# Optimization experiments

Measured on AMD Instinct MI355X. Metric: run time of the kernel, lower is better.

Reference implementation:

```python
import jax, jax.numpy as jnp
import numpy as np

B, RES, C = 4, 128, 256
HW = RES * RES
H_FFT, W_FFT = RES, RES // 2 + 1
NUM_BANDS, GATE_HIDDEN = 6, 128
LN_EPS = 1e-5
FFT_NORM = 'ortho'
INIT_RANGE = 0.02


def _band_info(h_fft, w_fft, nb):
    # static radial band partition of the rFFT2 plane (matches RadialBandGate.__init__)
    yy = np.arange(h_fft, dtype=np.float32)[:, None] / max(h_fft - 1, 1)
    xx = np.arange(w_fft, dtype=np.float32)[None, :] / max(w_fft - 1, 1)
    r = np.sqrt(yy ** 2 + xx ** 2)
    r = r / (r.max() + 1e-8)
    bid = np.minimum(np.floor(r * nb), nb - 1).astype(np.int32).reshape(-1)  # (F,)
    onehot = np.zeros((bid.size, nb), dtype=np.float32)
    onehot[np.arange(bid.size), bid] = 1.0
    counts = np.maximum(onehot.sum(0), 1.0)
    return jnp.asarray(bid), jnp.asarray(onehot), jnp.asarray(counts)

BAND_ID, BAND_ONEHOT, BAND_COUNTS = _band_info(H_FFT, W_FFT, NUM_BANDS)


def setup_inputs() -> dict:
    key = jax.random.key(0)
    ks = jax.random.split(key, 16)
    return {
        'x': jax.random.normal(ks[0], (B, HW, C), jnp.float32),
        'time': jax.random.uniform(ks[1], (B,), jnp.float32),
        'w_real': jax.random.normal(ks[2], (C, C), jnp.float32) * INIT_RANGE,
        'w_imag': jax.random.normal(ks[3], (C, C), jnp.float32) * INIT_RANGE,
        'conv_w': jax.random.normal(ks[4], (C, 1, 3, 3), jnp.float32) * 0.1,  # depthwise
        'lin_w': jax.random.normal(ks[5], (C, C), jnp.float32) * 0.02,
        'lin_b': jnp.zeros((C,), jnp.float32),
        'mlp_w1': jax.random.normal(ks[6], (GATE_HIDDEN, NUM_BANDS), jnp.float32) * 0.3,
        'mlp_b1': jnp.zeros((GATE_HIDDEN,), jnp.float32),
        'mlp_w2': jax.random.normal(ks[7], (NUM_BANDS, GATE_HIDDEN), jnp.float32) * 0.1,
        'mlp_b2': jnp.zeros((NUM_BANDS,), jnp.float32),
        'norm_ww': jax.random.normal(ks[8], (C, 1), jnp.float32) * 0.02,  # ConditionalLayerNorm.weight Linear(1,dim)
        'norm_wb': jnp.ones((C,), jnp.float32),
        'norm_bw': jax.random.normal(ks[9], (C, 1), jnp.float32) * 0.02,
        'norm_bb': jnp.zeros((C,), jnp.float32),
        'kx': jnp.asarray(0.25, jnp.float32),
        'ky': jnp.asarray(0.25, jnp.float32),
    }


def _band_gate(feat, mlp_w1, mlp_b1, mlp_w2, mlp_b2):
    # feat: (B, C, F) real. scatter-add per band via one-hot matmul, mean, MLP, gather back.
    sums = jnp.einsum('bcf,fn->bcn', feat, BAND_ONEHOT)           # (B,C,NB)
    means = sums / (BAND_COUNTS + 1e-6)
    h = jax.nn.relu(jnp.einsum('bcn,hn->bch', means, mlp_w1) + mlp_b1)
    alpha_band = jax.nn.sigmoid(jnp.einsum('bch,nh->bcn', h, mlp_w2) + mlp_b2)
    return alpha_band[:, :, BAND_ID]                               # (B,C,F)


def reference(x, time, w_real, w_imag, conv_w, lin_w, lin_b,
              mlp_w1, mlp_b1, mlp_w2, mlp_b2,
              norm_ww, norm_wb, norm_bw, norm_bb, kx, ky):
    h = w = RES
    x2 = jnp.transpose(x.reshape(B, h, w, C), (0, 3, 1, 2))        # (B,C,h,w)
    Xf = jnp.fft.rfft2(x2, norm=FFT_NORM)                          # (B,C,h_fft,w_fft) complex

    # low-frequency rectangular mask (int(sigmoid(k)*dim) == floor for positive values)
    kx_i = jnp.floor(jax.nn.sigmoid(kx) * H_FFT)
    ky_i = jnp.floor(jax.nn.sigmoid(ky) * W_FFT)
    mask = ((jnp.arange(H_FFT)[:, None] < kx_i) & (jnp.arange(W_FFT)[None, :] < ky_i))
    Xf_low = Xf * mask[None, None].astype(Xf.real.dtype)

    F = H_FFT * W_FFT
    Xf_low_flat = Xf_low.reshape(B, C, F)
    W = w_real + 1j * w_imag                                       # (C,C) complex
    Xf_low_mapped = jnp.einsum('cd,bdf->bcf', W, Xf_low_flat).reshape(B, C, H_FFT, W_FFT)

    Xf_high = Xf - Xf_low
    feat_pred = jnp.abs(jnp.abs(Xf_high).reshape(B, C, F) - jnp.abs(Xf_low).reshape(B, C, F))
    alpha = _band_gate(feat_pred, mlp_w1, mlp_b1, mlp_w2, mlp_b2).reshape(B, C, H_FFT, W_FFT)

    Xf_fused = alpha * Xf_low_mapped + (1.0 - alpha) * Xf_high
    x_spec = jnp.fft.irfft2(Xf_fused, s=(h, w), norm=FFT_NORM)     # (B,C,h,w) real

    # depthwise 3x3 conv, padding=1, no bias
    xl = jax.lax.conv_general_dilated(x2, conv_w, window_strides=(1, 1), padding='SAME',
                                      feature_group_count=C,
                                      dimension_numbers=('NCHW', 'OIHW', 'NCHW'))
    # pointwise linear over channel dim
    xc = jnp.transpose((x @ lin_w.T + lin_b).reshape(B, h, w, C), (0, 3, 1, 2))

    y = jnp.transpose(x_spec + xl + xc, (0, 2, 3, 1)).reshape(B, HW, C)

    # ConditionalLayerNorm
    mean = y.mean(axis=-1, keepdims=True)
    var = (y ** 2).mean(axis=-1, keepdims=True) - mean ** 2
    yn = (y - mean) / jnp.sqrt(var + LN_EPS)
    t = time.reshape(-1, 1)                                        # (B,1)
    weight = (t @ norm_ww.T + norm_wb)[:, None, :]                 # (B,1,C)
    bias = (t @ norm_bw.T + norm_bb)[:, None, :]
    return weight * yn + bias
```

## Files before the change

### kernel.cpp

```cpp
#include <hip/hip_runtime.h>
#include <math.h>

#define B_ 4
#define C_ 256
#define RES_ 128
#define HW_ 16384
#define WF_ 65
#define F_ 8320
#define FP_ 2880

typedef __attribute__((ext_vector_type(8))) short bf16x8;
typedef __attribute__((ext_vector_type(16))) float f32x16;

__device__ __forceinline__ int brev6(int j){ return (int)(__brev((unsigned)j) >> 26); }

__device__ __forceinline__ short f2bf(float f){
  unsigned u = __float_as_uint(f);
  unsigned r = (u + 0x7FFFu + ((u>>16)&1u)) >> 16;
  return (short)r;
}

__device__ __forceinline__ bf16x8 lds_frag(const short* p){
  union { bf16x8 v; int2 d[2]; } u;
  u.d[0] = *(const int2*)p;
  u.d[1] = *(const int2*)(p+4);
  return u.v;
}
__device__ __forceinline__ void lds_store8(short* p, bf16x8 v){
  union { bf16x8 v; int2 d[2]; } u; u.v = v;
  *(int2*)p = u.d[0]; *(int2*)(p+4) = u.d[1];
}

__device__ __forceinline__ int band_of(int row, int col){
  float yy = __fdiv_rn((float)row, 127.0f);
  float xx = __fdiv_rn((float)col, 64.0f);
  float rr = __fsqrt_rn(__fadd_rn(__fmul_rn(yy,yy), __fmul_rn(xx,xx)));
  float rm = __fadd_rn(__fsqrt_rn(2.0f), 1e-8f);
  float rn = __fdiv_rn(rr, rm);
  int b = (int)floorf(__fmul_rn(rn, 6.0f));
  return b > 5 ? 5 : b;
}

__device__ __forceinline__ float sigmoidf_(float v){ return 1.0f/(1.0f+expf(-v)); }

template<int SGN>
__device__ __forceinline__ float2 wave_fft64(float2 v, const float2* stw, int lane){
  #pragma unroll
  for (int s=0; s<6; s++){
    int H = 32 >> s;
    float ox = __shfl_xor(v.x, H);
    float oy = __shfl_xor(v.y, H);
    bool hi = (lane & H) != 0;
    float2 w = stw[s];
    float ws = (SGN < 0) ? -w.y : w.y;
    float sx = v.x + ox, sy = v.y + oy;
    float dx = ox - v.x, dy = oy - v.y;
    float rx = dx*w.x - dy*ws;
    float ry = dx*ws + dy*w.x;
    v.x = hi ? rx : sx;
    v.y = hi ? ry : sy;
  }
  return v;
}

__device__ __forceinline__ void make_stage_tw(float2* stw, int lane){
  #pragma unroll
  for (int s=0; s<6; s++){
    int H = 32 >> s;
    int t = (lane & (H-1)) << s;
    float sn, cs;
    sincosf(6.283185307179586f*(float)t/64.0f, &sn, &cs);
    stw[s] = make_float2(cs, sn);
  }
}

__device__ __forceinline__ void redist2(float2 a0, float2 a1, int lane, float2& u0, float2& u1){
  int s0 = lane >> 1, s1 = s0 + 32;
  bool odd = (lane & 1) != 0;
  float t0x = __shfl(a0.x, s0), t0y = __shfl(a0.y, s0);
  float t1x = __shfl(a1.x, s0), t1y = __shfl(a1.y, s0);
  u0 = odd ? make_float2(t1x, t1y) : make_float2(t0x, t0y);
  float q0x = __shfl(a0.x, s1), q0y = __shfl(a0.y, s1);
  float q1x = __shfl(a1.x, s1), q1y = __shfl(a1.y, s1);
  u1 = odd ? make_float2(q1x, q1y) : make_float2(q0x, q0y);
}

__global__ __launch_bounds__(256) void k_transpose(const float* __restrict__ x, float* __restrict__ x2){
  __shared__ float tile[64][68];
  int b = blockIdx.z;
  int hw0 = blockIdx.x*64, c0 = blockIdx.y*64;
  int tid = threadIdx.x;
  #pragma unroll
  for (int q=0;q<4;q++){
    int p = tid + q*256;
    int hw = p >> 4, c4 = (p & 15) << 2;
    float4 v = *(const float4*)&x[((size_t)b*HW_ + hw0 + hw)*C_ + c0 + c4];
    *(float4*)&tile[hw][c4] = v;
  }
  __syncthreads();
  #pragma unroll
  for (int q=0;q<4;q++){
    int p = tid + q*256;
    int c = p >> 4, h4 = (p & 15) << 2;
    float4 v = make_float4(tile[h4][c], tile[h4+1][c], tile[h4+2][c], tile[h4+3][c]);
    *(float4*)&x2[((size_t)b*C_ + c0 + c)*HW_ + hw0 + h4] = v;
  }
}

__global__ __launch_bounds__(256) void k_counts(float* __restrict__ counts, unsigned char* __restrict__ bid_t){
  int tid = threadIdx.x;
  float acc[6] = {0,0,0,0,0,0};
  for (int p = tid; p < F_; p += 256){
    int kx = p >> 7, ky = p & 127;
    int bnd = band_of(ky, kx);
    bid_t[p] = (unsigned char)bnd;
    #pragma unroll
    for (int n=0;n<6;n++) acc[n] += (bnd==n) ? 1.0f : 0.0f;
  }
  __shared__ float red[6][256];
  #pragma unroll
  for (int n=0;n<6;n++) red[n][tid] = acc[n];
  __syncthreads();
  for (int s=128; s>0; s>>=1){
    if (tid < s){
      #pragma unroll
      for (int n=0;n<6;n++) red[n][tid] += red[n][tid+s];
    }
    __syncthreads();
  }
  if (tid < 6) counts[tid] = fmaxf(red[tid][0], 1.0f);
}

__global__ __launch_bounds__(256) void k_wbf16(const float* __restrict__ wre, const float* __restrict__ wim,
                                               const float* __restrict__ lw,
                                               short* __restrict__ Wre, short* __restrict__ Wim,
                                               short* __restrict__ WL){
  int c = blockIdx.x, tid = threadIdx.x, plane = blockIdx.y;
  int idx = c*C_ + tid;
  if (plane == 0)      Wre[idx] = f2bf(wre[idx]);
  else if (plane == 1) Wim[idx] = f2bf(wim[idx]);
  else                 WL[idx]  = f2bf(lw[idx]);
}

__global__ __launch_bounds__(512) void k_fwd(const float* __restrict__ x2, float2* __restrict__ Xft,
                                             const float* __restrict__ counts, const unsigned char* __restrict__ bid_t,
                                             const float* __restrict__ w1, const float* __restrict__ b1,
                                             const float* __restrict__ w2, const float* __restrict__ b2,
                                             float* __restrict__ alpha){
  __shared__ float2 lt[65*129];
  __shared__ float red[6][8];
  __shared__ float means[6], h[128];
  int tid = threadIdx.x;
  int lane = tid & 63, wv = tid >> 6;
  float2 stw[6];
  make_stage_tw(stw, lane);
  float sn128, cs128;
  sincosf(6.283185307179586f*(float)lane/128.0f, &sn128, &cs128);
  int slice = blockIdx.x;
  const float* img = x2 + (size_t)slice*HW_;
  #pragma unroll
  for (int i=0; i<16; i++){
    int rr = wv*16 + i;
    float2 y = *(const float2*)(img + rr*128 + lane*2);
    float2 v = wave_fft64<-1>(y, stw, lane);
    int rbk = brev6(lane);
    float2 Yk; Yk.x = __shfl(v.x, rbk); Yk.y = __shfl(v.y, rbk);
    int rbm = brev6((64 - lane) & 63);
    float2 Ym; Ym.x = __shfl(v.x, rbm); Ym.y = __shfl(v.y, rbm);
    float sx = Yk.x + Ym.x, sy = Yk.y - Ym.y;
    float dx = Yk.x - Ym.x, dy = Yk.y + Ym.y;
    lt[lane*129 + rr] = make_float2(0.5f*(sx - sn128*dx + cs128*dy),
                                    0.5f*(sy - cs128*dx - sn128*dy));
    if (lane == 0)
      lt[64*129 + rr] = make_float2(Yk.x - Yk.y, 0.0f);
  }
  __syncthreads();
  float2* xout = Xft + (size_t)slice*F_;
  float acc[6] = {0,0,0,0,0,0};
  for (int kx = wv; kx < 65; kx += 8){
    float2 a0 = lt[kx*129 + (lane<<1)];
    float2 a1 = lt[kx*129 + (lane<<1) + 1];
    float2 u0, u1;
    redist2(a0, a1, lane, u0, u1);
    float2 s = make_float2(u0.x+u1.x, u0.y+u1.y);
    float ddx = u0.x-u1.x, ddy = u0.y-u1.y;
    float2 dw = make_float2(ddx*cs128 + ddy*sn128, ddy*cs128 - ddx*sn128);
    float2 v0 = wave_fft64<-1>(s, stw, lane);
    float2 v1 = wave_fft64<-1>(dw, stw, lane);
    int rb = brev6(lane);
    float ex = __shfl(v0.x, rb), ey = __shfl(v0.y, rb);
    float ox = __shfl(v1.x, rb), oy = __shfl(v1.y, rb);
    ex *= 0.0078125f; ey *= 0.0078125f;
    ox *= 0.0078125f; oy *= 0.0078125f;
    *(float4*)(xout + (size_t)kx*128 + (lane<<1)) = make_float4(ex, ey, ox, oy);
    float me = __fsqrt_rn(ex*ex + ey*ey);
    float mo = __fsqrt_rn(ox*ox + oy*oy);
    int be = (int)bid_t[kx*128 + (lane<<1)];
    int bo = (int)bid_t[kx*128 + (lane<<1) + 1];
    #pragma unroll
    for (int n=0;n<6;n++) acc[n] += ((be==n) ? me : 0.0f) + ((bo==n) ? mo : 0.0f);
  }
  #pragma unroll
  for (int n=0;n<6;n++){
    float v = acc[n];
    #pragma unroll
    for (int off=32; off>0; off>>=1) v += __shfl_xor(v, off);
    if (lane == 0) red[n][wv] = v;
  }
  __syncthreads();
  if (tid < 6){
    float t = 0.0f;
    #pragma unroll
    for (int q=0;q<8;q++) t += red[tid][q];
    means[tid] = t / (counts[tid] + 1e-6f);
  }
  __syncthreads();
  if (tid < 128){
    float hv = b1[tid];
    #pragma unroll
    for (int n=0;n<6;n++) hv += means[n]*w1[tid*6+n];
    h[tid] = fmaxf(hv, 0.0f);
  }
  __syncthreads();
  if (tid < 6){
    float o = b2[tid];
    for (int j=0;j<128;j++) o += h[j]*w2[tid*128+j];
    alpha[slice*6 + tid] = sigmoidf_(o);
  }
}

__global__ __launch_bounds__(256) void k_xt(const float2* __restrict__ Xft,
                                            short* __restrict__ XtRe, short* __restrict__ XtIm){
  __shared__ short sre[72*130];
  __shared__ short sim[72*130];
  int tid = threadIdx.x;
  int kx = blockIdx.x, d0 = blockIdx.y*128, b = blockIdx.z;
  const float2* xb = Xft + ((size_t)(b*C_ + d0))*F_ + (size_t)kx*128;
  for (int p = tid; p < 72*128; p += 256){
    int d = p / 72, ky = p - d*72;
    float2 v = xb[(size_t)d*F_ + ky];
    sre[ky*130 + d] = f2bf(v.x);
    sim[ky*130 + d] = f2bf(v.y);
  }
  __syncthreads();
  short* dre = XtRe + ((size_t)b*FP_ + (size_t)kx*72)*C_ + d0;
  short* dim_ = XtIm + ((size_t)b*FP_ + (size_t)kx*72)*C_ + d0;
  for (int p = tid; p < 72*128; p += 256){
    int ky = p >> 7, d = p & 127;
    dre[(size_t)ky*C_ + d] = sre[ky*130 + d];
    dim_[(size_t)ky*C_ + d] = sim[ky*130 + d];
  }
}

__global__ __launch_bounds__(256) void k_mix_mfma(const short* __restrict__ Wre, const short* __restrict__ Wim,
                                                  const short* __restrict__ XtRe, const short* __restrict__ XtIm,
                                                  const float* __restrict__ kxp, const float* __restrict__ kyp,
                                                  float2* __restrict__ mappedP){
  __shared__ short Are[64][36], Aim[64][36], Bre[64][36], Bim[64][36];
  int tid = threadIdx.x;
  int fp0 = blockIdx.x*64, c0 = blockIdx.y*64, b = blockIdx.z;
  int lane = tid & 63, w = tid >> 6;
  int mt = (w >> 1)*32, nt = (w & 1)*32;
  f32x16 accre = {0.f,0.f,0.f,0.f,0.f,0.f,0.f,0.f,0.f,0.f,0.f,0.f,0.f,0.f,0.f,0.f};
  f32x16 accim = {0.f,0.f,0.f,0.f,0.f,0.f,0.f,0.f,0.f,0.f,0.f,0.f,0.f,0.f,0.f,0.f};
  const short* xrb = XtRe + ((size_t)b*FP_ + fp0)*C_;
  const short* xib = XtIm + ((size_t)b*FP_ + fp0)*C_;
  int row4 = tid >> 2, part = tid & 3;
  for (int kc=0; kc<8; kc++){
    int d0 = kc*32;
    __syncthreads();
    lds_store8(&Are[row4][part*8], *(const bf16x8*)&Wre[(c0+row4)*C_ + d0 + part*8]);
    lds_store8(&Aim[row4][part*8], *(const bf16x8*)&Wim[(c0+row4)*C_ + d0 + part*8]);
    lds_store8(&Bre[row4][part*8], *(const bf16x8*)&xrb[(size_t)row4*C_ + d0 + part*8]);
    lds_store8(&Bim[row4][part*8], *(const bf16x8*)&xib[(size_t)row4*C_ + d0 + part*8]);
    __syncthreads();
    #pragma unroll
    for (int ks=0; ks<2; ks++){
      int koff = ks*16 + (lane>>5)*8;
      bf16x8 are = lds_frag(&Are[mt + (lane&31)][koff]);
      bf16x8 aim = lds_frag(&Aim[mt + (lane&31)][koff]);
      bf16x8 bre = lds_frag(&Bre[nt + (lane&31)][koff]);
      bf16x8 bim = lds_frag(&Bim[nt + (lane&31)][koff]);
      bf16x8 naim;
      { union { bf16x8 v; unsigned u[4]; } t1, t2; t1.v = aim;
        #pragma unroll
        for (int j=0;j<4;j++) t2.u[j] = t1.u[j] ^ 0x80008000u;
        naim = t2.v; }
      accre = __builtin_amdgcn_mfma_f32_32x32x16_bf16(are,  bre, accre, 0,0,0);
      accre = __builtin_amdgcn_mfma_f32_32x32x16_bf16(naim, bim, accre, 0,0,0);
      accim = __builtin_amdgcn_mfma_f32_32x32x16_bf16(are,  bim, accim, 0,0,0);
      accim = __builtin_amdgcn_mfma_f32_32x32x16_bf16(aim,  bre, accim, 0,0,0);
    }
  }
  float rowlim = floorf(sigmoidf_(kxp[0])*128.0f);
  float collim = floorf(sigmoidf_(kyp[0])*65.0f);
  int n = fp0 + nt + (lane & 31);
  int ky = n % 72, kx = n / 72;
  bool live = ((float)ky < rowlim) && ((float)kx < collim);
  #pragma unroll
  for (int reg=0; reg<16; reg++){
    int r = (reg & 3) + 8*(reg >> 2) + 4*(lane >> 5);
    int c = c0 + mt + r;
    if (live)
      mappedP[((size_t)(b*C_ + c))*FP_ + n] = make_float2(accre[reg], accim[reg]);
  }
}

__global__ __launch_bounds__(256) void k_pw_mfma(const float* __restrict__ x, const short* __restrict__ WL,
                                                  const float* __restrict__ lb, float* __restrict__ xcs){
  __shared__ short As[64][36], Bs[64][36];
  int tid = threadIdx.x;
  int hw0 = blockIdx.x*64, c0 = blockIdx.y*64, b = blockIdx.z;
  int lane = tid & 63, w = tid >> 6;
  int mt = (w >> 1)*32, nt = (w & 1)*32;
  f32x16 acc = {0.f,0.f,0.f,0.f,0.f,0.f,0.f,0.f,0.f,0.f,0.f,0.f,0.f,0.f,0.f,0.f};
  const float* xb = x + ((size_t)b*HW_ + hw0)*C_;
  int row4 = tid >> 2, part = tid & 3;
  for (int kc=0; kc<8; kc++){
    int d0 = kc*32;
    __syncthreads();
    lds_store8(&As[row4][part*8], *(const bf16x8*)&WL[(c0+row4)*C_ + d0 + part*8]);
    {
      const float* src = &xb[(size_t)row4*C_ + d0 + part*8];
      float4 va = *(const float4*)src;
      float4 vb = *(const float4*)(src+4);
      bf16x8 bv;
      bv[0]=f2bf(va.x); bv[1]=f2bf(va.y); bv[2]=f2bf(va.z); bv[3]=f2bf(va.w);
      bv[4]=f2bf(vb.x); bv[5]=f2bf(vb.y); bv[6]=f2bf(vb.z); bv[7]=f2bf(vb.w);
      lds_store8(&Bs[row4][part*8], bv);
    }
    __syncthreads();
    #pragma unroll
    for (int ks=0; ks<2; ks++){
      int koff = ks*16 + (lane>>5)*8;
      bf16x8 a  = lds_frag(&As[mt + (lane&31)][koff]);
      bf16x8 bb = lds_frag(&Bs[nt + (lane&31)][koff]);
      acc = __builtin_amdgcn_mfma_f32_32x32x16_bf16(a, bb, acc, 0,0,0);
    }
  }
  int n = hw0 + nt + (lane & 31);
  #pragma unroll
  for (int reg=0; reg<16; reg++){
    int r = (reg & 3) + 8*(reg >> 2) + 4*(lane >> 5);
    int c = c0 + mt + r;
    xcs[((size_t)(b*C_ + c))*HW_ + n] = acc[reg] + lb[c];
  }
}

__global__ __launch_bounds__(512) void k_inv(const float2* __restrict__ Xft, const float2* __restrict__ mappedP,
                                             const float* __restrict__ alpha, const unsigned char* __restrict__ bid_t,
                                             const float* __restrict__ kxp, const float* __restrict__ kyp,
                                             const float* __restrict__ xcs, const float* __restrict__ x2,
                                             const float* __restrict__ cw, float* __restrict__ sbuf){
  __shared__ float2 lt[65*129];
  __shared__ float al[6];
  int tid = threadIdx.x;
  int lane = tid & 63, wv = tid >> 6;
  float2 stw[6];
  make_stage_tw(stw, lane);
  float sn128, cs128;
  sincosf(6.283185307179586f*(float)lane/128.0f, &sn128, &cs128);
  int slice = blockIdx.x;
  int ch = slice & 255;
  if (tid < 6) al[tid] = alpha[slice*6 + tid];
  float rowlim = floorf(sigmoidf_(kxp[0])*128.0f);
  float collim = floorf(sigmoidf_(kyp[0])*65.0f);
  const float* img = x2 + (size_t)slice*HW_;
  int base = wv*16;
  float2 rows[18];
  #pragma unroll
  for (int i=0;i<18;i++){
    int gr = base - 1 + i;
    rows[i] = ((unsigned)gr < 128u) ? *(const float2*)(img + (size_t)gr*128 + (lane<<1))
                                    : make_float2(0.0f, 0.0f);
  }
  float w9[9];
  #pragma unroll
  for (int k=0;k<9;k++) w9[k] = cw[ch*9+k];
  __syncthreads();
  const float2* xfb = Xft + (size_t)slice*F_;
  const float2* mpb = mappedP + (size_t)slice*FP_;
  for (int kx = wv; kx < 65; kx += 8){
    float4 rv = *(const float4*)(xfb + (size_t)kx*128 + (lane<<1));
    int ky0 = lane << 1;
    float a_e = al[(int)bid_t[kx*128 + ky0]];
    float a_o = al[(int)bid_t[kx*128 + ky0 + 1]];
    bool cok  = ((float)kx < collim);
    bool in_e = cok && ((float)ky0 < rowlim);
    bool in_o = cok && ((float)(ky0+1) < rowlim);
    float2 ve, vo;
    if (in_e){
      float4 mv = *(const float4*)(mpb + (size_t)kx*72 + ky0);
      ve = make_float2(mv.x*a_e, mv.y*a_e);
      vo = in_o ? make_float2(mv.z*a_o, mv.w*a_o)
                : make_float2(rv.z*(1.0f-a_o), rv.w*(1.0f-a_o));
    } else {
      ve = make_float2(rv.x*(1.0f-a_e), rv.y*(1.0f-a_e));
      vo = make_float2(rv.z*(1.0f-a_o), rv.w*(1.0f-a_o));
    }
    float2 u0, u1;
    redist2(ve, vo, lane, u0, u1);
    float2 s = make_float2(u0.x+u1.x, u0.y+u1.y);
    float ddx = u0.x-u1.x, ddy = u0.y-u1.y;
    float2 dw = make_float2(ddx*cs128 - ddy*sn128, ddx*sn128 + ddy*cs128);
    float2 v0 = wave_fft64<1>(s, stw, lane);
    float2 v1 = wave_fft64<1>(dw, stw, lane);
    int rb = brev6(lane);
    float2 z0; z0.x = __shfl(v0.x, rb); z0.y = __shfl(v0.y, rb);
    float2 z1; z1.x = __shfl(v1.x, rb); z1.y = __shfl(v1.y, rb);
    lt[kx*129 + ky0]     = z0;
    lt[kx*129 + ky0 + 1] = z1;
  }
  __syncthreads();
  size_t gbase = (size_t)slice*HW_;
  #pragma unroll
  for (int i=0;i<16;i++){
    int row = base + i;
    float2 a = lt[lane*129 + row];
    float2 b = lt[(64-lane)*129 + row];
    if (lane == 0){ a.y = 0.0f; b.y = 0.0f; }
    float sx = a.x + b.x, sy = a.y - b.y;
    float dx = a.x - b.x, dy = a.y + b.y;
    float2 yk = make_float2(0.5f*(sx - sn128*dx - cs128*dy),
                            0.5f*(sy + cs128*dx - sn128*dy));
    float2 v = wave_fft64<1>(yk, stw, lane);
    int rbk = brev6(lane);
    float2 z; z.x = __shfl(v.x, rbk); z.y = __shfl(v.y, rbk);
    int xx = lane << 1;
    float c0 = 0.0f, c1 = 0.0f;
    #pragma unroll
    for (int dy2=0; dy2<3; dy2++){
      float2 cv = rows[i + dy2];
      float l = __shfl_up(cv.y, 1);
      if (lane == 0) l = 0.0f;
      float r = __shfl_down(cv.x, 1);
      if (lane == 63) r = 0.0f;
      c0 += l*w9[dy2*3+0] + cv.x*w9[dy2*3+1] + cv.y*w9[dy2*3+2];
      c1 += cv.x*w9[dy2*3+0] + cv.y*w9[dy2*3+1] + r*w9[dy2*3+2];
    }
    size_t g = gbase + (size_t)(row*128 + xx);
    float2 xc = *(const float2*)&xcs[g];
    float2 o;
    o.x = z.x*0.015625f + xc.x + c0;
    o.y = z.y*0.015625f + xc.y + c1;
    *(float2*)&sbuf[g] = o;
  }
}

__global__ __launch_bounds__(256) void k_norm(const float* __restrict__ sbuf, const float* __restrict__ timev,
                                              const float* __restrict__ nww, const float* __restrict__ nwb,
                                              const float* __restrict__ nbw, const float* __restrict__ nbb,
                                              float* __restrict__ out){
  __shared__ float tile[64][65];
  __shared__ float p1[64][5], p2[64][5];
  __shared__ float mv[64], rv[64], wv_[256], bv_[256];
  int b = blockIdx.y, hw0 = blockIdx.x*64;
  int tid = threadIdx.x;
  {
    float t = timev[b];
    wv_[tid] = t*nww[tid] + nwb[tid];
    bv_[tid] = t*nbw[tid] + nbb[tid];
  }
  int hwl = tid & 63, cg = tid >> 6;
  const float* p = sbuf + (size_t)b*C_*HW_ + hw0 + hwl;
  float s1 = 0.0f, s2 = 0.0f;
  for (int c = cg*64; c < cg*64 + 64; c++){
    float v = p[(size_t)c*HW_];
    s1 += v; s2 += v*v;
  }
  p1[hwl][cg] = s1; p2[hwl][cg] = s2;
  __syncthreads();
  if (tid < 64){
    float t1 = p1[tid][0] + p1[tid][1] + p1[tid][2] + p1[tid][3];
    float t2 = p2[tid][0] + p2[tid][1] + p2[tid][2] + p2[tid][3];
    float mean = t1 * (1.0f/256.0f);
    float var  = t2 * (1.0f/256.0f) - mean*mean;
    mv[tid] = mean;
    rv[tid] = 1.0f / sqrtf(var + 1e-5f);
  }
  __syncthreads();
  for (int cg2=0; cg2<4; cg2++){
    int c0 = cg2*64;
    #pragma unroll
    for (int q=0;q<16;q++){
      int pp = tid + q*256;
      int cl = pp >> 6, hl = pp & 63;
      tile[cl][hl] = sbuf[((size_t)(b*C_ + c0 + cl))*HW_ + hw0 + hl];
    }
    __syncthreads();
    #pragma unroll
    for (int q=0;q<16;q++){
      int pp = tid + q*256;
      int hl = pp >> 6, cl = pp & 63;
      float v = tile[cl][hl];
      out[((size_t)(b*HW_ + hw0 + hl))*C_ + c0 + cl] = wv_[c0+cl]*((v - mv[hl])*rv[hl]) + bv_[c0+cl];
    }
    __syncthreads();
  }
}

extern "C" void kernel_launch(void* const* d_in, const int* in_sizes, int n_in,
                              void* d_out, int out_size, void* d_ws, size_t ws_size,
                              hipStream_t stream){
  const float* x      = (const float*)d_in[0];
  const float* timev  = (const float*)d_in[1];
  const float* w_real = (const float*)d_in[2];
  const float* w_imag = (const float*)d_in[3];
  const float* conv_w = (const float*)d_in[4];
  const float* lin_w  = (const float*)d_in[5];
  const float* lin_b  = (const float*)d_in[6];
  const float* mlp_w1 = (const float*)d_in[7];
  const float* mlp_b1 = (const float*)d_in[8];
  const float* mlp_w2 = (const float*)d_in[9];
  const float* mlp_b2 = (const float*)d_in[10];
  const float* norm_ww= (const float*)d_in[11];
  const float* norm_wb= (const float*)d_in[12];
  const float* norm_bw= (const float*)d_in[13];
  const float* norm_bb= (const float*)d_in[14];
  const float* kxp    = (const float*)d_in[15];
  const float* kyp    = (const float*)d_in[16];

  float* ws = (float*)d_ws;
  float*  alpha  = ws;
  unsigned char* bid_t = (unsigned char*)(ws + 6144);
  float*  counts = ws + 8224;
  short*  Wre_bf = (short*)(ws + 139360);
  short*  Wim_bf = (short*)(ws + 172128);
  short*  WL_bf  = (short*)(ws + 204896);
  float*  x2     = ws + 237664;
  float2* Xft    = (float2*)(ws + 17014880);
  float*  CbF    = ws + 34054240;
  short*  XtRe   = (short*)CbF;
  short*  XtIm   = (short*)(CbF + 1474560);
  float2* mappedP= (float2*)(CbF + 2949120);
  float*  sb     = CbF + 8847360;
  float*  xcs    = (float*)d_out;
  float*  out    = (float*)d_out;

  k_transpose    <<<dim3(256, 4, B_), 256, 0, stream>>>(x, x2);
  k_counts       <<<1, 256, 0, stream>>>(counts, bid_t);
  k_wbf16        <<<dim3(256, 3), 256, 0, stream>>>(w_real, w_imag, lin_w, Wre_bf, Wim_bf, WL_bf);
  k_fwd          <<<1024, 512, 0, stream>>>(x2, Xft, counts, bid_t, mlp_w1, mlp_b1, mlp_w2, mlp_b2, alpha);
  k_xt           <<<dim3(40, 2, B_), 256, 0, stream>>>(Xft, XtRe, XtIm);
  k_pw_mfma      <<<dim3(256, 4, B_), 256, 0, stream>>>(x, WL_bf, lin_b, xcs);
  k_mix_mfma     <<<dim3(45, 4, B_), 256, 0, stream>>>(Wre_bf, Wim_bf, XtRe, XtIm, kxp, kyp, mappedP);
  k_inv          <<<1024, 512, 0, stream>>>(Xft, mappedP, alpha, bid_t, kxp, kyp, xcs, x2, conv_w, sb);
  k_norm         <<<dim3(256, B_), 256, 0, stream>>>(sb, timev, norm_ww, norm_wb, norm_bw, norm_bb, out);
}
```

Baseline: 424.1 us.

## Split inverse FFT kernel into column pass and row-tiled pass

The fused inverse kernel held a 65x129 float2 LDS transpose tile per 512-thread block. It is now split into two kernels. A column kernel writes its FFT results in place back to the Xft buffer in global memory, and a row kernel processes 32-row tiles with a much smaller LDS tile, 4x more blocks and a higher occupancy hint. The aim is better occupancy and parallelism, paid for with an extra global round trip of the spectrum and one more launch.

```diff
diff --git a/kernel.cpp b/kernel.cpp
--- a/kernel.cpp
+++ b/kernel.cpp
@@ -347,40 +347,24 @@
   }
 }
 
-__global__ __launch_bounds__(512) void k_inv(const float2* __restrict__ Xft, const float2* __restrict__ mappedP,
-                                             const float* __restrict__ alpha, const unsigned char* __restrict__ bid_t,
-                                             const float* __restrict__ kxp, const float* __restrict__ kyp,
-                                             const float* __restrict__ xcs, const float* __restrict__ x2,
-                                             const float* __restrict__ cw, float* __restrict__ sbuf){
-  __shared__ float2 lt[65*129];
+__global__ __launch_bounds__(256) void k_inv_cols(float2* __restrict__ XftY, const float2* __restrict__ mappedP,
+                                                  const float* __restrict__ alpha, const unsigned char* __restrict__ bid_t,
+                                                  const float* __restrict__ kxp, const float* __restrict__ kyp){
   __shared__ float al[6];
   int tid = threadIdx.x;
   int lane = tid & 63, wv = tid >> 6;
+  int slice = blockIdx.x;
   float2 stw[6];
   make_stage_tw(stw, lane);
   float sn128, cs128;
   sincosf(6.283185307179586f*(float)lane/128.0f, &sn128, &cs128);
-  int slice = blockIdx.x;
-  int ch = slice & 255;
   if (tid < 6) al[tid] = alpha[slice*6 + tid];
   float rowlim = floorf(sigmoidf_(kxp[0])*128.0f);
   float collim = floorf(sigmoidf_(kyp[0])*65.0f);
-  const float* img = x2 + (size_t)slice*HW_;
-  int base = wv*16;
-  float2 rows[18];
-  #pragma unroll
-  for (int i=0;i<18;i++){
-    int gr = base - 1 + i;
-    rows[i] = ((unsigned)gr < 128u) ? *(const float2*)(img + (size_t)gr*128 + (lane<<1))
-                                    : make_float2(0.0f, 0.0f);
-  }
-  float w9[9];
-  #pragma unroll
-  for (int k=0;k<9;k++) w9[k] = cw[ch*9+k];
-  __syncthreads();
-  const float2* xfb = Xft + (size_t)slice*F_;
+  __syncthreads();
+  float2* xfb = XftY + (size_t)slice*F_;
   const float2* mpb = mappedP + (size_t)slice*FP_;
-  for (int kx = wv; kx < 65; kx += 8){
+  for (int kx = wv; kx < 65; kx += 4){
     float4 rv = *(const float4*)(xfb + (size_t)kx*128 + (lane<<1));
     int ky0 = lane << 1;
     float a_e = al[(int)bid_t[kx*128 + ky0]];
@@ -406,18 +390,50 @@
     float2 v0 = wave_fft64<1>(s, stw, lane);
     float2 v1 = wave_fft64<1>(dw, stw, lane);
     int rb = brev6(lane);
-    float2 z0; z0.x = __shfl(v0.x, rb); z0.y = __shfl(v0.y, rb);
-    float2 z1; z1.x = __shfl(v1.x, rb); z1.y = __shfl(v1.y, rb);
-    lt[kx*129 + ky0]     = z0;
-    lt[kx*129 + ky0 + 1] = z1;
-  }
-  __syncthreads();
-  size_t gbase = (size_t)slice*HW_;
-  #pragma unroll
-  for (int i=0;i<16;i++){
-    int row = base + i;
-    float2 a = lt[lane*129 + row];
-    float2 b = lt[(64-lane)*129 + row];
+    float4 outv;
+    outv.x = __shfl(v0.x, rb); outv.y = __shfl(v0.y, rb);
+    outv.z = __shfl(v1.x, rb); outv.w = __shfl(v1.y, rb);
+    *(float4*)(xfb + (size_t)kx*128 + (lane<<1)) = outv;
+  }
+}
+
+__global__ __launch_bounds__(256,6) void k_inv_rows(const float2* __restrict__ Y1t, const float* __restrict__ xcs,
+                                                    const float* __restrict__ x2, const float* __restrict__ cw,
+                                                    float* __restrict__ sbuf){
+  __shared__ float2 ytile[65*33];
+  int tid = threadIdx.x;
+  int lane = tid & 63, wv = tid >> 6;
+  float2 stw[6];
+  make_stage_tw(stw, lane);
+  float sn128, cs128;
+  sincosf(6.283185307179586f*(float)lane/128.0f, &sn128, &cs128);
+  int slice = blockIdx.x >> 2;
+  int ch = slice & 255;
+  int r0 = (blockIdx.x & 3) * 32;
+  const float* img = x2 + (size_t)slice*HW_;
+  int base = r0 + wv*8;
+  float2 rows[10];
+  #pragma unroll
+  for (int i=0;i<10;i++){
+    int gr = base - 1 + i;
+    rows[i] = ((unsigned)gr < 128u) ? *(const float2*)(img + (size_t)gr*128 + (lane<<1))
+                                    : make_float2(0.0f, 0.0f);
+  }
+  const float2* ysrc = Y1t + (size_t)slice*F_ + r0;
+  for (int p = tid; p < 65*32; p += 256){
+    int kx = p >> 5, rr = p & 31;
+    ytile[kx*33 + rr] = ysrc[(size_t)kx*128 + rr];
+  }
+  float w9[9];
+  #pragma unroll
+  for (int k=0;k<9;k++) w9[k] = cw[ch*9+k];
+  __syncthreads();
+  size_t gbase = (size_t)slice*HW_ + (size_t)r0*128;
+  #pragma unroll
+  for (int i=0;i<8;i++){
+    int row = wv*8 + i;
+    float2 a = ytile[lane*33 + row];
+    float2 b = ytile[(64-lane)*33 + row];
     if (lane == 0){ a.y = 0.0f; b.y = 0.0f; }
     float sx = a.x + b.x, sy = a.y - b.y;
     float dx = a.x - b.x, dy = a.y + b.y;
@@ -544,6 +560,7 @@
   k_xt           <<<dim3(40, 2, B_), 256, 0, stream>>>(Xft, XtRe, XtIm);
   k_pw_mfma      <<<dim3(256, 4, B_), 256, 0, stream>>>(x, WL_bf, lin_b, xcs);
   k_mix_mfma     <<<dim3(45, 4, B_), 256, 0, stream>>>(Wre_bf, Wim_bf, XtRe, XtIm, kxp, kyp, mappedP);
-  k_inv          <<<1024, 512, 0, stream>>>(Xft, mappedP, alpha, bid_t, kxp, kyp, xcs, x2, conv_w, sb);
+  k_inv_cols     <<<1024, 256, 0, stream>>>(Xft, mappedP, alpha, bid_t, kxp, kyp);
+  k_inv_rows     <<<4096, 256, 0, stream>>>((const float2*)Xft, xcs, x2, conv_w, sb);
   k_norm         <<<dim3(256, B_), 256, 0, stream>>>(sb, timev, norm_ww, norm_wb, norm_bw, norm_bb, out);
 }
```

Result: slower. 441.5 us (+4.1%).
